# Kernel optimization log

Measured on AMD Instinct MI355X. Metric: run time of the kernel, lower is better.

The kernel has to match this reference:

```python
import jax, jax.numpy as jnp
import numpy as np

NUM_HEADS = 8  # from init_kwargs


def setup_inputs() -> dict:
    key = jax.random.key(0)
    ks = jax.random.split(key, 8)
    B, N, Din, H, Dout, E = 4, 2048, 256, 512, 256, 65536
    s = 0.02
    return {
        "x": jax.random.normal(ks[0], (B, N, Din), jnp.float32),
        "edge_index": jax.random.randint(ks[1], (2, E), 0, N),
        "W_gcn": jax.random.normal(ks[2], (Din, H), jnp.float32) * s,
        "b_gcn": jnp.zeros((H,), jnp.float32),
        "in_proj_w": jax.random.normal(ks[3], (3 * H, H), jnp.float32) * s,
        "in_proj_b": jnp.zeros((3 * H,), jnp.float32),
        "out_proj_w": jax.random.normal(ks[4], (H, H), jnp.float32) * s,
        "out_proj_b": jnp.zeros((H,), jnp.float32),
        "fc_w": jax.random.normal(ks[5], (H, Dout), jnp.float32) * s,
        "fc_b": jnp.zeros((Dout,), jnp.float32),
    }


def _gcn(x, edge_index, W, b):
    # PyG GCNConv: add self-loops, symmetric normalization, gather-scatter aggregation.
    B, N, _ = x.shape
    loop = jnp.arange(N)
    src = jnp.concatenate([edge_index[0], loop])  # message source j
    dst = jnp.concatenate([edge_index[1], loop])  # aggregation target i
    deg = jnp.zeros((N,), x.dtype).at[dst].add(1.0)
    dinv = jnp.where(deg > 0, jax.lax.rsqrt(deg), 0.0)
    norm = dinv[src] * dinv[dst]                  # [Etot]
    xl = x @ W                                    # [B, N, H]
    msgs = xl[:, src, :] * norm[None, :, None]    # [B, Etot, H]
    out = jnp.zeros_like(xl).at[:, dst].add(msgs)  # scatter-add over edges
    return out + b


def _mha(x_nbh, wi, bi, wo, bo, nh):
    # torch MultiheadAttention, input [N(seq), B, H], self-attention.
    N, B, H = x_nbh.shape
    dh = H // nh
    qkv = x_nbh @ wi.T + bi                       # [N, B, 3H]
    q, k, v = jnp.split(qkv, 3, axis=-1)
    q = q.reshape(N, B, nh, dh) * (dh ** -0.5)
    k = k.reshape(N, B, nh, dh)
    v = v.reshape(N, B, nh, dh)
    scores = jnp.einsum("nbhd,mbhd->bhnm", q, k)  # [B, nh, N, N]
    attn = jax.nn.softmax(scores, axis=-1)
    o = jnp.einsum("bhnm,mbhd->nbhd", attn, v).reshape(N, B, H)
    return o @ wo.T + bo


def reference(x, edge_index, W_gcn, b_gcn, in_proj_w, in_proj_b,
              out_proj_w, out_proj_b, fc_w, fc_b):
    h = _gcn(x, edge_index, W_gcn, b_gcn)         # [B, N, H]
    h = jnp.transpose(h, (1, 0, 2))               # [N, B, H]
    h = _mha(h, in_proj_w, in_proj_b, out_proj_w, out_proj_b, NUM_HEADS)
    h = jnp.transpose(h, (1, 0, 2))               # [B, N, H]
    h = jax.nn.relu(h)
    return h @ fc_w + fc_b                        # [B, N, Dout]
```

## Files before the change

kernel.cpp:

```cpp
#include <hip/hip_runtime.h>
#include <hip/hip_bf16.h>


#define NN 2048
#define HH 512
#define NHEAD 8
#define DH 64

typedef _Float16 f16;
typedef __attribute__((ext_vector_type(2))) _Float16 f16x2;
typedef __attribute__((ext_vector_type(4))) _Float16 f16x4;
typedef __attribute__((ext_vector_type(8))) _Float16 f16x8;
typedef __attribute__((ext_vector_type(2))) __fp16 fp16v2;
typedef __attribute__((ext_vector_type(4))) float f32x4;

#define GLOAD_LDS16(g, l)                                              \
  __builtin_amdgcn_global_load_lds(                                    \
      (const __attribute__((address_space(1))) void*)(g),              \
      (__attribute__((address_space(3))) void*)(l), 16, 0, 0)


__global__ __launch_bounds__(256) void prep_cvt_kernel(const float* __restrict__ wi,
                                                       const float* __restrict__ wo,
                                                       f16* __restrict__ wi16,
                                                       f16* __restrict__ wo16,
                                                       float* __restrict__ deg,
                                                       int* __restrict__ cursor) {
  const int bid = blockIdx.x, t = threadIdx.x;
  if (bid < 768) {
    const int i = bid * 256 + t;
    const float4 v = ((const float4*)wi)[i];
    f16x4 o = { (f16)v.x, (f16)v.y, (f16)v.z, (f16)v.w };
    ((f16x4*)wi16)[i] = o;
  } else if (bid < 1024) {
    const int i = (bid - 768) * 256 + t;
    const float4 v = ((const float4*)wo)[i];
    f16x4 o = { (f16)v.x, (f16)v.y, (f16)v.z, (f16)v.w };
    ((f16x4*)wo16)[i] = o;
  } else {
    for (int i = t; i < NN; i += 256) { deg[i] = 1.0f; cursor[i] = 0; }
  }
}

__global__ __launch_bounds__(256) void prep_transpose_kernel(const float* __restrict__ wg,
                                                             const float* __restrict__ fcw,
                                                             f16* __restrict__ wg16t,
                                                             f16* __restrict__ fcw16t) {
  __shared__ float tbuf[32][33];
  const float* in;
  f16* outp;
  int R, C, bx, by;
  if (blockIdx.x < 128) { in = wg;  outp = wg16t;  R = 256; C = 512;
                          bx = blockIdx.x & 15; by = blockIdx.x >> 4; }
  else { int id = blockIdx.x - 128; in = fcw; outp = fcw16t; R = 512; C = 256;
         bx = id & 7; by = id >> 3; }
  const int c0 = bx * 32, r0 = by * 32;
  const int tx = threadIdx.x & 31, ty = threadIdx.x >> 5;
#pragma unroll
  for (int i = 0; i < 32; i += 8) tbuf[ty + i][tx] = in[(size_t)(r0 + ty + i) * C + c0 + tx];
  __syncthreads();
#pragma unroll
  for (int i = 0; i < 32; i += 8)
    outp[(size_t)(c0 + ty + i) * R + r0 + tx] = (f16)tbuf[tx][ty + i];
}


__global__ __launch_bounds__(256) void count_deg_kernel(const int* __restrict__ ei, int E,
                                                        float* __restrict__ deg) {
  int e = blockIdx.x * 256 + threadIdx.x;
  if (e < E) atomicAdd(&deg[ei[E + e]], 1.0f);
}

__global__ __launch_bounds__(1024) void build_rowptr_kernel(const float* __restrict__ deg,
                                                            float* __restrict__ dinv,
                                                            int* __restrict__ rowptr) {
  __shared__ int a[NN];
  __shared__ int bbuf[NN];
  const int t = threadIdx.x;
  for (int i = t; i < NN; i += 1024) {
    float dg = deg[i];
    a[i] = (int)dg - 1;
    dinv[i] = rsqrtf(dg);
  }
  __syncthreads();
  int* src = a;
  int* dst = bbuf;
  for (int off = 1; off < NN; off <<= 1) {
    for (int i = t; i < NN; i += 1024) {
      int v = src[i];
      if (i >= off) v += src[i - off];
      dst[i] = v;
    }
    __syncthreads();
    int* tmp = src; src = dst; dst = tmp;
  }
  for (int i = t; i < NN; i += 1024) rowptr[i + 1] = src[i];
  if (t == 0) rowptr[0] = 0;
}

__global__ __launch_bounds__(256) void fill_csr_kernel(const int* __restrict__ ei, int E,
                                                       const int* __restrict__ rowptr,
                                                       int* __restrict__ cursor,
                                                       int* __restrict__ csr_src) {
  int e = blockIdx.x * 256 + threadIdx.x;
  if (e < E) {
    int s = ei[e];
    int d = ei[E + e];
    int pos = atomicAdd(&cursor[d], 1);
    csr_src[rowptr[d] + pos] = s;
  }
}


template <int OUTMODE, bool BIAS, bool RELU, bool AF32, int MT = 128>
__global__ __launch_bounds__(256) void mfma_gemm_kernel(
    const void* __restrict__ Ap, const f16* __restrict__ Bt,
    const float* __restrict__ bias, void* __restrict__ Cout,
    int M, int N, int K,
    f16* __restrict__ q_out, f16* __restrict__ k_out, f16* __restrict__ v_out) {
  constexpr int MI = MT / 32;
  __shared__ f16 As[MT * 32];
  __shared__ f16 Bs[128 * 32];
  const int tid = threadIdx.x;
  const int wave = tid >> 6, lane = tid & 63;
  const int quad = lane >> 4, l16 = lane & 15;
  const int m0 = blockIdx.y * MT, n0 = blockIdx.x * 128;
  const int moff = (wave >> 1) * (MI * 16), noff = (wave & 1) * 64;

  f32x4 acc[MI][4];
#pragma unroll
  for (int i = 0; i < MI; ++i)
#pragma unroll
    for (int j = 0; j < 4; ++j) acc[i][j] = (f32x4){0.f, 0.f, 0.f, 0.f};

  const int rpw = MT / 4;
  const int srowA = rpw * wave + (lane >> 2);
  const int srowB = 32 * wave + (lane >> 2);
  const int kch = (lane & 3) * 8;
  const f16* Ag = (const f16*)Ap + (size_t)(m0 + srowA) * K + kch;
  const float* Ag32 = (const float*)Ap + (size_t)(m0 + srowA) * K + kch;
  const f16* Bg = Bt + (size_t)(n0 + srowB) * K + kch;
  f16* As_w = &As[(rpw * wave) * 32];
  f16* Bs_w = &Bs[(32 * wave) * 32];

  for (int k0 = 0; k0 < K; k0 += 32) {
    __syncthreads();
    if (AF32) {
#pragma unroll
      for (int t = 0; t < (MT == 128 ? 2 : 1); ++t) {
        const float* g = Ag32 + k0 + (size_t)(16 * t) * K;
        const float4 u0 = *(const float4*)g;
        const float4 u1 = *(const float4*)(g + 4);
        f16x8 o = { (f16)u0.x, (f16)u0.y, (f16)u0.z, (f16)u0.w,
                    (f16)u1.x, (f16)u1.y, (f16)u1.z, (f16)u1.w };
        *(f16x8*)&As[(srowA + 16 * t) * 32 + kch] = o;
      }
    } else {
      GLOAD_LDS16(Ag + k0, As_w);
      if (MT == 128) GLOAD_LDS16(Ag + k0 + (size_t)16 * K, As_w + 16 * 32);
    }
    GLOAD_LDS16(Bg + k0, Bs_w);
    GLOAD_LDS16(Bg + k0 + (size_t)16 * K, Bs_w + 16 * 32);
    __syncthreads();
    f16x8 af[MI], bf[4];
#pragma unroll
    for (int m16 = 0; m16 < MI; ++m16)
      af[m16] = *(const f16x8*)&As[(moff + m16 * 16 + l16) * 32 + quad * 8];
#pragma unroll
    for (int n16 = 0; n16 < 4; ++n16)
      bf[n16] = *(const f16x8*)&Bs[(noff + n16 * 16 + l16) * 32 + quad * 8];
#pragma unroll
    for (int m16 = 0; m16 < MI; ++m16)
#pragma unroll
      for (int n16 = 0; n16 < 4; ++n16)
        acc[m16][n16] =
            __builtin_amdgcn_mfma_f32_16x16x32_f16(af[m16], bf[n16], acc[m16][n16], 0, 0, 0);
  }

  float bv[4];
#pragma unroll
  for (int n16 = 0; n16 < 4; ++n16)
    bv[n16] = BIAS ? bias[n0 + noff + n16 * 16 + l16] : 0.f;

  if (OUTMODE == 2) {
    const int hblk = (n0 >> 6) + (wave & 1);
    const int which = hblk >> 3, h = hblk & 7;
    f16* dst = (which == 0) ? q_out : (which == 1) ? k_out : v_out;
    const float scale = (which == 0) ? 0.125f * 1.44269504f : 1.0f;
#pragma unroll
    for (int m16 = 0; m16 < MI; ++m16) {
#pragma unroll
      for (int r = 0; r < 4; ++r) {
        const int m = m0 + moff + m16 * 16 + quad * 4 + r;
        const int b = m >> 11, ns = m & 2047;
        f16* row = dst + ((size_t)(b * 8 + h) * NN + ns) * DH;
#pragma unroll
        for (int n16 = 0; n16 < 4; ++n16) {
          const int d = n16 * 16 + l16;
          row[d] = (f16)((acc[m16][n16][r] + bv[n16]) * scale);
        }
      }
    }
  } else {
#pragma unroll
    for (int m16 = 0; m16 < MI; ++m16) {
#pragma unroll
      for (int r = 0; r < 4; ++r) {
        const size_t row = (size_t)(m0 + moff + m16 * 16 + quad * 4 + r) * N;
#pragma unroll
        for (int n16 = 0; n16 < 4; ++n16) {
          const int col = n0 + noff + n16 * 16 + l16;
          float v = acc[m16][n16][r] + bv[n16];
          if (RELU) v = fmaxf(v, 0.f);
          if (OUTMODE == 0) ((float*)Cout)[row + col] = v;
          else ((f16*)Cout)[row + col] = (f16)v;
        }
      }
    }
  }
}


__global__ __launch_bounds__(256) void gcn_aggregate_kernel(const f16* __restrict__ xl,
                                                            const float* __restrict__ dinv,
                                                            const int* __restrict__ rowptr,
                                                            const int* __restrict__ csr_src,
                                                            const float* __restrict__ b_gcn,
                                                            f16* __restrict__ out) {
  __shared__ int s_src[256];
  __shared__ float s_dv[256];
  const int i = blockIdx.x;
  const int tid = threadIdx.x;
  const int b = tid >> 6;
  const int f = (tid & 63) * 8;
  const float dv_i = dinv[i];
  const f16* xb = xl + (size_t)b * NN * HH;
  float acc[8];
  {
    const f16x8 self = *(const f16x8*)&xb[(size_t)i * HH + f];
#pragma unroll
    for (int c = 0; c < 8; ++c) acc[c] = (float)self[c] * dv_i;
  }
  const int beg = rowptr[i], end = rowptr[i + 1];
  for (int c0 = beg; c0 < end; c0 += 256) {
    const int cnt = min(256, end - c0);
    __syncthreads();
    if (tid < cnt) {
      int s = csr_src[c0 + tid];
      s_src[tid] = s;
      s_dv[tid] = dinv[s];
    }
    __syncthreads();
    for (int t = 0; t < cnt; ++t) {
      const f16x8 v = *(const f16x8*)&xb[(size_t)s_src[t] * HH + f];
      const float w = s_dv[t];
#pragma unroll
      for (int c = 0; c < 8; ++c) acc[c] = fmaf((float)v[c], w, acc[c]);
    }
  }
  const float4 bg0 = *(const float4*)&b_gcn[f];
  const float4 bg1 = *(const float4*)&b_gcn[f + 4];
  f16x8 o;
  o[0] = (f16)(acc[0] * dv_i + bg0.x);
  o[1] = (f16)(acc[1] * dv_i + bg0.y);
  o[2] = (f16)(acc[2] * dv_i + bg0.z);
  o[3] = (f16)(acc[3] * dv_i + bg0.w);
  o[4] = (f16)(acc[4] * dv_i + bg1.x);
  o[5] = (f16)(acc[5] * dv_i + bg1.y);
  o[6] = (f16)(acc[6] * dv_i + bg1.z);
  o[7] = (f16)(acc[7] * dv_i + bg1.w);
  *(f16x8*)&out[((size_t)b * NN + i) * HH + f] = o;
}


__global__ __launch_bounds__(256) void flash_attn_f16_kernel(const f16* __restrict__ Qb,
                                                             const f16* __restrict__ Kb,
                                                             const f16* __restrict__ Vb,
                                                             f16* __restrict__ out) {
  const int LDK = 72;
  const int LDV = 136;
  __shared__ f16 Ks[128 * LDK];
  __shared__ f16 Vt[64 * LDV];
  const int tid = threadIdx.x;
  const int wave = tid >> 6, lane = tid & 63;
  const int quad = lane >> 4, l16 = lane & 15;
  const int n0 = blockIdx.x * 128;
  const int bh = blockIdx.y;
  const int b = bh >> 3, h = bh & 7;
  const f16* kb = Kb + (size_t)bh * NN * DH;
  const f16* vb = Vb + (size_t)bh * NN * DH;

  f16x8 aq[2][2];
#pragma unroll
  for (int g = 0; g < 2; ++g) {
    const f16* qf = Qb + ((size_t)bh * NN + n0 + (wave + 4 * g) * 16 + l16) * DH + quad * 8;
    aq[g][0] = *(const f16x8*)qf;
    aq[g][1] = *(const f16x8*)(qf + 32);
  }

  float l_part[2] = {0.f, 0.f};
  f32x4 acc_o[2][4];
#pragma unroll
  for (int g = 0; g < 2; ++g)
#pragma unroll
    for (int n16 = 0; n16 < 4; ++n16) acc_o[g][n16] = (f32x4){0.f, 0.f, 0.f, 0.f};

  const int vdg = tid & 15, jbb = tid >> 4;

  for (int kt = 0; kt < NN / 128; ++kt) {
    const int k0 = kt * 128;
    __syncthreads();
#pragma unroll
    for (int i = 0; i < 4; ++i) {
      int idx = tid + 256 * i;
      int r = idx >> 3, koff = (idx & 7) * 8;
      *(f16x8*)&Ks[r * LDK + koff] = *(const f16x8*)(kb + (size_t)(k0 + r) * DH + koff);
    }
#pragma unroll
    for (int cc = 0; cc < 2; ++cc) {
      const int jb = jbb + 16 * cc;
      const int sb4 = (jb >> 3) * 32 + (jb & 3) * 8 + ((jb >> 2) & 1) * 4;
      f16x4 vv[4];
#pragma unroll
      for (int i = 0; i < 4; ++i)
        vv[i] = *(const f16x4*)(vb + (size_t)(k0 + jb * 4 + i) * DH + vdg * 4);
#pragma unroll
      for (int c = 0; c < 4; ++c) {
        f16x4 o = { vv[0][c], vv[1][c], vv[2][c], vv[3][c] };
        *(f16x4*)&Vt[(vdg * 4 + c) * LDV + sb4] = o;
      }
    }
    __syncthreads();
#pragma unroll
    for (int p = 0; p < 4; ++p) {
      f32x4 sA[2][2];
#pragma unroll
      for (int t = 0; t < 2; ++t) {
        const f16x8 ak0 = *(const f16x8*)&Ks[(p * 32 + t * 16 + l16) * LDK + quad * 8];
        const f16x8 ak1 = *(const f16x8*)&Ks[(p * 32 + t * 16 + l16) * LDK + quad * 8 + 32];
#pragma unroll
        for (int g = 0; g < 2; ++g) {
          f32x4 s = {0.f, 0.f, 0.f, 0.f};
          s = __builtin_amdgcn_mfma_f32_16x16x32_f16(ak0, aq[g][0], s, 0, 0, 0);
          s = __builtin_amdgcn_mfma_f32_16x16x32_f16(ak1, aq[g][1], s, 0, 0, 0);
          sA[g][t] = s;
        }
      }
      f16x8 bvv[4];
#pragma unroll
      for (int n16 = 0; n16 < 4; ++n16)
        bvv[n16] = *(const f16x8*)&Vt[(n16 * 16 + l16) * LDV + p * 32 + quad * 8];
#pragma unroll
      for (int g = 0; g < 2; ++g) {
        float e[8];
        float sum = 0.f;
#pragma unroll
        for (int t = 0; t < 2; ++t)
#pragma unroll
          for (int r = 0; r < 4; ++r) {
            const float v = exp2f(sA[g][t][r]);
            e[t * 4 + r] = v;
            sum += v;
          }
        l_part[g] += sum;
        union { f16x8 v8; fp16v2 p2[4]; } ap;
#pragma unroll
        for (int c = 0; c < 4; ++c)
          ap.p2[c] = __builtin_amdgcn_cvt_pkrtz(e[2 * c], e[2 * c + 1]);
#pragma unroll
        for (int n16 = 0; n16 < 4; ++n16)
          acc_o[g][n16] = __builtin_amdgcn_mfma_f32_16x16x32_f16(ap.v8, bvv[n16], acc_o[g][n16], 0, 0, 0);
      }
    }
  }
#pragma unroll
  for (int g = 0; g < 2; ++g) {
    float lp = l_part[g];
    lp += __shfl_xor(lp, 16);
    lp += __shfl_xor(lp, 32);
    f16* obase = out + ((size_t)b * NN + n0 + (wave + 4 * g) * 16) * HH + h * DH;
#pragma unroll
    for (int r = 0; r < 4; ++r) {
      const float lr = __shfl(lp, (lane & 48) | (quad * 4 + r));
      const float inv = 1.0f / lr;
#pragma unroll
      for (int n16 = 0; n16 < 4; ++n16)
        obase[(size_t)(quad * 4 + r) * HH + n16 * 16 + l16] = (f16)(acc_o[g][n16][r] * inv);
    }
  }
}


extern "C" void kernel_launch(void* const* d_in, const int* in_sizes, int n_in,
                              void* d_out, int out_size, void* d_ws, size_t ws_size,
                              hipStream_t stream) {
  const float* x     = (const float*)d_in[0];
  const int*   ei    = (const int*)d_in[1];
  const float* W_gcn = (const float*)d_in[2];
  const float* b_gcn = (const float*)d_in[3];
  const float* wi    = (const float*)d_in[4];
  const float* bi    = (const float*)d_in[5];
  const float* wo    = (const float*)d_in[6];
  const float* bo    = (const float*)d_in[7];
  const float* fcw   = (const float*)d_in[8];
  const float* fcb   = (const float*)d_in[9];
  float* out = (float*)d_out;
  const int E = in_sizes[1] / 2;
  const int M = 4 * NN;

  char* wsb = (char*)d_ws;
  const size_t MB = 1u << 20;
  f16* xl16   = (f16*)(wsb + 4 * MB);
  f16* hb16   = (f16*)(wsb + 12 * MB);
  f16* Qb     = (f16*)(wsb + 20 * MB);
  f16* Kb     = (f16*)(wsb + 28 * MB);
  f16* Vb     = (f16*)(wsb + 36 * MB);
  f16* attn16 = (f16*)(wsb + 44 * MB);
  f16* proj16 = (f16*)(wsb + 52 * MB);
  f16* wi16   = (f16*)(wsb + 60 * MB);
  f16* wo16   = (f16*)(wsb + 62 * MB);
  f16* wg16t  = (f16*)(wsb + 63 * MB);
  f16* fcw16t = (f16*)(wsb + 64 * MB);
  float* deg  = (float*)(wsb + 65 * MB);
  float* dinv = deg + NN;
  int* rowptr = (int*)(dinv + NN);
  int* cursor = rowptr + 2080;
  int* csr    = cursor + NN;

  prep_cvt_kernel<<<1025, 256, 0, stream>>>(wi, wo, wi16, wo16, deg, cursor);
  prep_transpose_kernel<<<256, 256, 0, stream>>>(W_gcn, fcw, wg16t, fcw16t);

  count_deg_kernel<<<(E + 255) / 256, 256, 0, stream>>>(ei, E, deg);
  build_rowptr_kernel<<<1, 1024, 0, stream>>>(deg, dinv, rowptr);
  fill_csr_kernel<<<(E + 255) / 256, 256, 0, stream>>>(ei, E, rowptr, cursor, csr);

  mfma_gemm_kernel<1, false, false, true, 64><<<dim3(4, 128), 256, 0, stream>>>(
      x, wg16t, nullptr, xl16, M, 512, 256, nullptr, nullptr, nullptr);
  gcn_aggregate_kernel<<<NN, 256, 0, stream>>>(xl16, dinv, rowptr, csr, b_gcn, hb16);
  mfma_gemm_kernel<2, true, false, false><<<dim3(12, 64), 256, 0, stream>>>(
      hb16, wi16, bi, nullptr, M, 1536, 512, Qb, Kb, Vb);
  flash_attn_f16_kernel<<<dim3(NN / 128, 32), 256, 0, stream>>>(Qb, Kb, Vb, attn16);
  mfma_gemm_kernel<1, true, true, false, 64><<<dim3(4, 128), 256, 0, stream>>>(
      attn16, wo16, bo, proj16, M, 512, 512, nullptr, nullptr, nullptr);
  mfma_gemm_kernel<0, true, false, false, 64><<<dim3(2, 128), 256, 0, stream>>>(
      proj16, fcw16t, fcb, out, M, 256, 512, nullptr, nullptr, nullptr);
}
```

Before: 262.0 us.

## Prefetch next K/V tile into registers and remap flash-attention block order

The flash attention loop now loads the next K and V tile from global memory into registers while the current tile is being computed, so load latency overlaps the MFMA work. Block indices are remapped so that consecutive blocks cover different batch-head pairs rather than consecutive query tiles. The softmax probabilities are also converted to f16 directly instead of through packed round-toward-zero conversions. Holding the prefetched tile in registers raises register pressure, which may lower occupancy.

Result: no change. 261.8 us (-0.1%).

```diff
diff --git a/kernel.cpp b/kernel.cpp
--- a/kernel.cpp
+++ b/kernel.cpp
@@ -11,7 +11,6 @@
 typedef __attribute__((ext_vector_type(2))) _Float16 f16x2;
 typedef __attribute__((ext_vector_type(4))) _Float16 f16x4;
 typedef __attribute__((ext_vector_type(8))) _Float16 f16x8;
-typedef __attribute__((ext_vector_type(2))) __fp16 fp16v2;
 typedef __attribute__((ext_vector_type(4))) float f32x4;
 
 #define GLOAD_LDS16(g, l)                                              \
@@ -284,8 +283,9 @@
   const int tid = threadIdx.x;
   const int wave = tid >> 6, lane = tid & 63;
   const int quad = lane >> 4, l16 = lane & 15;
-  const int n0 = blockIdx.x * 128;
-  const int bh = blockIdx.y;
+  const int lin = blockIdx.x + 16 * blockIdx.y;
+  const int bh = lin & 31;
+  const int n0 = (lin >> 5) * 128;
   const int b = bh >> 3, h = bh & 7;
   const f16* kb = Kb + (size_t)bh * NN * DH;
   const f16* vb = Vb + (size_t)bh * NN * DH;
@@ -306,28 +306,47 @@
     for (int n16 = 0; n16 < 4; ++n16) acc_o[g][n16] = (f32x4){0.f, 0.f, 0.f, 0.f};
 
   const int vdg = tid & 15, jbb = tid >> 4;
+  const int krow = tid >> 1, kcol = (tid & 1) * 32;
+
+  f16x8 kreg[4];
+  f16x4 vreg[2][4];
+#pragma unroll
+  for (int i = 0; i < 4; ++i)
+    kreg[i] = *(const f16x8*)(kb + (size_t)krow * DH + kcol + 8 * i);
+#pragma unroll
+  for (int cc = 0; cc < 2; ++cc) {
+    const int jb = jbb + 16 * cc;
+#pragma unroll
+    for (int i = 0; i < 4; ++i)
+      vreg[cc][i] = *(const f16x4*)(vb + (size_t)(jb * 4 + i) * DH + vdg * 4);
+  }
 
   for (int kt = 0; kt < NN / 128; ++kt) {
-    const int k0 = kt * 128;
-    __syncthreads();
-#pragma unroll
-    for (int i = 0; i < 4; ++i) {
-      int idx = tid + 256 * i;
-      int r = idx >> 3, koff = (idx & 7) * 8;
-      *(f16x8*)&Ks[r * LDK + koff] = *(const f16x8*)(kb + (size_t)(k0 + r) * DH + koff);
-    }
+    __syncthreads();
+#pragma unroll
+    for (int i = 0; i < 4; ++i)
+      *(f16x8*)&Ks[krow * LDK + kcol + 8 * i] = kreg[i];
 #pragma unroll
     for (int cc = 0; cc < 2; ++cc) {
       const int jb = jbb + 16 * cc;
       const int sb4 = (jb >> 3) * 32 + (jb & 3) * 8 + ((jb >> 2) & 1) * 4;
-      f16x4 vv[4];
+#pragma unroll
+      for (int c = 0; c < 4; ++c) {
+        f16x4 o = { vreg[cc][0][c], vreg[cc][1][c], vreg[cc][2][c], vreg[cc][3][c] };
+        *(f16x4*)&Vt[(vdg * 4 + c) * LDV + sb4] = o;
+      }
+    }
+    if (kt + 1 < NN / 128) {
+      const int k1 = (kt + 1) * 128;
 #pragma unroll
       for (int i = 0; i < 4; ++i)
-        vv[i] = *(const f16x4*)(vb + (size_t)(k0 + jb * 4 + i) * DH + vdg * 4);
-#pragma unroll
-      for (int c = 0; c < 4; ++c) {
-        f16x4 o = { vv[0][c], vv[1][c], vv[2][c], vv[3][c] };
-        *(f16x4*)&Vt[(vdg * 4 + c) * LDV + sb4] = o;
+        kreg[i] = *(const f16x8*)(kb + (size_t)(k1 + krow) * DH + kcol + 8 * i);
+#pragma unroll
+      for (int cc = 0; cc < 2; ++cc) {
+        const int jb = jbb + 16 * cc;
+#pragma unroll
+        for (int i = 0; i < 4; ++i)
+          vreg[cc][i] = *(const f16x4*)(vb + (size_t)(k1 + jb * 4 + i) * DH + vdg * 4);
       }
     }
     __syncthreads();
@@ -352,24 +371,20 @@
         bvv[n16] = *(const f16x8*)&Vt[(n16 * 16 + l16) * LDV + p * 32 + quad * 8];
 #pragma unroll
       for (int g = 0; g < 2; ++g) {
-        float e[8];
+        f16x8 ap;
         float sum = 0.f;
 #pragma unroll
         for (int t = 0; t < 2; ++t)
 #pragma unroll
           for (int r = 0; r < 4; ++r) {
             const float v = exp2f(sA[g][t][r]);
-            e[t * 4 + r] = v;
             sum += v;
+            ap[t * 4 + r] = (f16)v;
           }
         l_part[g] += sum;
-        union { f16x8 v8; fp16v2 p2[4]; } ap;
-#pragma unroll
-        for (int c = 0; c < 4; ++c)
-          ap.p2[c] = __builtin_amdgcn_cvt_pkrtz(e[2 * c], e[2 * c + 1]);
 #pragma unroll
         for (int n16 = 0; n16 < 4; ++n16)
-          acc_o[g][n16] = __builtin_amdgcn_mfma_f32_16x16x32_f16(ap.v8, bvv[n16], acc_o[g][n16], 0, 0, 0);
+          acc_o[g][n16] = __builtin_amdgcn_mfma_f32_16x16x32_f16(ap, bvv[n16], acc_o[g][n16], 0, 0, 0);
       }
     }
   }
@@ -439,7 +454,7 @@
   gcn_aggregate_kernel<<<NN, 256, 0, stream>>>(xl16, dinv, rowptr, csr, b_gcn, hb16);
   mfma_gemm_kernel<2, true, false, false><<<dim3(12, 64), 256, 0, stream>>>(
       hb16, wi16, bi, nullptr, M, 1536, 512, Qb, Kb, Vb);
-  flash_attn_f16_kernel<<<dim3(NN / 128, 32), 256, 0, stream>>>(Qb, Kb, Vb, attn16);
+  flash_attn_f16_kernel<<<dim3(16, 32), 256, 0, stream>>>(Qb, Kb, Vb, attn16);
   mfma_gemm_kernel<1, true, true, false, 64><<<dim3(4, 128), 256, 0, stream>>>(
       attn16, wo16, bo, proj16, M, 512, 512, nullptr, nullptr, nullptr);
   mfma_gemm_kernel<0, true, false, false, 64><<<dim3(2, 128), 256, 0, stream>>>(
```
